# Kernel tuning notes

Hardware: AMD Instinct MI355X
Metric: run time of the kernel (lower is better)

## Reference

```python
import jax, jax.numpy as jnp
import numpy as np

S, B, H, T = 1024, 32, 1024, 512


def setup_inputs() -> dict:
    key = jax.random.key(0)
    ks = jax.random.split(key, 7)
    scale = 1.0 / np.sqrt(H)
    return {
        "hidden": jax.random.normal(ks[0], (S, B, H), dtype=jnp.float32),
        "x": jax.random.normal(ks[1], (B, T, H), dtype=jnp.float32),
        "problem_q": jax.random.normal(ks[2], (B, H), dtype=jnp.float32),
        "K_w": jax.random.normal(ks[3], (H, H), dtype=jnp.float32) * scale,
        "K_b": jax.random.normal(ks[4], (H,), dtype=jnp.float32) * scale,
        "V_w": jax.random.normal(ks[5], (H, H), dtype=jnp.float32) * scale,
        "V_b": jax.random.normal(ks[6], (H,), dtype=jnp.float32) * scale,
    }


def reference(hidden, x, problem_q, K_w, K_b, V_w, V_b):
    # hidden: [S, B, H] -> hidden2: [B, S, H]
    hidden2 = jnp.transpose(hidden, (1, 0, 2))
    # Linear projections (torch Linear: y = x @ W.T + b)
    k = jnp.einsum("bsh,kh->bsk", hidden2, K_w) + K_b  # [B, S, H]
    v = jnp.einsum("bsh,kh->bsk", hidden2, V_w) + V_b  # [B, S, H]
    # scores[b,t,s] = x[b,t] . k[b,s]  (QK^T per batch)
    scores = jnp.einsum("bth,bsh->bts", x, k)
    attn = jax.nn.softmax(scores, axis=-1)  # softmax over encoder positions S
    out = jax.nn.sigmoid(jnp.einsum("bts,bsh->bth", attn, v))  # [B, T, H]
    return out
```

## Files before the change

kernel.cpp:

```cpp
#include <hip/hip_runtime.h>

typedef unsigned short u16;
typedef __attribute__((ext_vector_type(8))) short short8;
typedef __attribute__((ext_vector_type(4))) float f32x4;
typedef __attribute__((ext_vector_type(4))) u16 u16x4;
typedef __attribute__((ext_vector_type(4))) unsigned int u32x4;

#define DEVINL static __device__ __forceinline__

DEVINL u16 f2bf(float f) {
  unsigned u = __builtin_bit_cast(unsigned, f);
  u += 0x7fffu + ((u >> 16) & 1u);
  return (u16)(u >> 16);
}
DEVINL float bf2f(u16 h) {
  return __builtin_bit_cast(float, ((unsigned)h) << 16);
}

DEVINL void gload16(const void* g, void* l) {
  __builtin_amdgcn_global_load_lds(
      (const __attribute__((address_space(1))) void*)g,
      (__attribute__((address_space(3))) void*)l, 16, 0, 0);
}

#define BAR() asm volatile("s_barrier" ::: "memory")
#define WAIT_VM0() asm volatile("s_waitcnt vmcnt(0)" ::: "memory")
#define WAIT_LGKM0() asm volatile("s_waitcnt lgkmcnt(0)" ::: "memory")


__global__ __launch_bounds__(256) void cvt_hidden3_k(const float* __restrict__ hid,
                                                     u16* __restrict__ hhi,
                                                     u16* __restrict__ hlo,
                                                     u16* __restrict__ hT) {
  __shared__ u16 tl[64][72];
  const int s0 = blockIdx.x * 64;
  const int h0 = blockIdx.y * 64;
  const int b = blockIdx.z;
  const int t = threadIdx.x;
  const int r = t >> 4;
  const int c4 = (t & 15) * 4;
#pragma unroll
  for (int it = 0; it < 4; ++it) {
    const int s = it * 16 + r;
    const f32x4 v = *(const f32x4*)(hid + ((size_t)(s0 + s) * 32 + b) * 1024 + h0 + c4);
    u16x4 oh, ol;
#pragma unroll
    for (int j = 0; j < 4; ++j) {
      const u16 hv = f2bf(v[j]);
      oh[j] = hv;
      ol[j] = f2bf(v[j] - bf2f(hv));
      tl[s][c4 + j] = hv;
    }
    const size_t base = ((size_t)b * 1024 + s0 + s) * 1024 + h0 + c4;
    *(u16x4*)(hhi + base) = oh;
    *(u16x4*)(hlo + base) = ol;
  }
  __syncthreads();
  const int h = t >> 2;
  const int sq = (t & 3) * 16;
  u16 tmp[16] __attribute__((aligned(16)));
#pragma unroll
  for (int i = 0; i < 16; ++i) tmp[i] = tl[sq + i][h];
  u16* dst = hT + ((size_t)b * 1024 + h0 + h) * 1024 + s0 + sq;
  *(u32x4*)(dst) = *(const u32x4*)&tmp[0];
  *(u32x4*)(dst + 8) = *(const u32x4*)&tmp[8];
}

__global__ __launch_bounds__(256) void cvt_split_k(const float* __restrict__ in,
                                                   u16* __restrict__ hi_o,
                                                   u16* __restrict__ lo_o, long n4) {
  long i = (long)blockIdx.x * 256 + threadIdx.x;
  const long stride = (long)gridDim.x * 256;
  for (; i < n4; i += stride) {
    const f32x4 v = ((const f32x4*)in)[i];
    u16x4 oh, ol;
#pragma unroll
    for (int j = 0; j < 4; ++j) {
      const u16 hi = f2bf(v[j]);
      oh[j] = hi;
      ol[j] = f2bf(v[j] - bf2f(hi));
    }
    ((u16x4*)hi_o)[i] = oh;
    ((u16x4*)lo_o)[i] = ol;
  }
}

__global__ __launch_bounds__(256) void cvt_f32_bf16_k(const float* __restrict__ in,
                                                      u16* __restrict__ out, long n4) {
  long i = (long)blockIdx.x * 256 + threadIdx.x;
  const long stride = (long)gridDim.x * 256;
  for (; i < n4; i += stride) {
    const f32x4 v = ((const f32x4*)in)[i];
    u16x4 o;
#pragma unroll
    for (int j = 0; j < 4; ++j) o[j] = f2bf(v[j]);
    ((u16x4*)out)[i] = o;
  }
}

__global__ __launch_bounds__(256) void cvt_w_split_t_k(const float* __restrict__ in,
                                                       u16* __restrict__ hi_o,
                                                       u16* __restrict__ lo_o) {
  __shared__ float tile[64][65];
  const int bh = blockIdx.x * 64;
  const int bj = blockIdx.y * 64;
  const int t = threadIdx.x;
  const int r = t >> 4;
  const int c4 = (t & 15) * 4;
#pragma unroll
  for (int it = 0; it < 4; ++it) {
    const int row = it * 16 + r;
    const f32x4 v = *(const f32x4*)(in + (size_t)(bj + row) * 1024 + bh + c4);
#pragma unroll
    for (int j = 0; j < 4; ++j) tile[c4 + j][row] = v[j];
  }
  __syncthreads();
#pragma unroll
  for (int it = 0; it < 4; ++it) {
    const int hrow = it * 16 + r;
    u16x4 oh, ol;
#pragma unroll
    for (int j = 0; j < 4; ++j) {
      const float f = tile[hrow][c4 + j];
      const u16 hv = f2bf(f);
      oh[j] = hv;
      ol[j] = f2bf(f - bf2f(hv));
    }
    *(u16x4*)(hi_o + (size_t)(bh + hrow) * 1024 + bj + c4) = oh;
    *(u16x4*)(lo_o + (size_t)(bh + hrow) * 1024 + bj + c4) = ol;
  }
}

template <int CMODE>
__global__ __launch_bounds__(512) void gemm3_8ph_k(
    const u16* __restrict__ Ah_, const u16* __restrict__ Al_,
    const u16* __restrict__ Bh_, const u16* __restrict__ Bl_,
    void* __restrict__ C0, void* __restrict__ C1) {
  __shared__ u16 lds[2][2][256 * 64];
  const int bid = blockIdx.x;
  const int swz = (bid & 7) * 32 + (bid >> 3);
  int m0, n0;
  const u16 *Ah, *Al, *Bh, *Bl;
  float* Cf = nullptr;
  u16 *Chi = nullptr, *Clo = nullptr;
  if (CMODE == 0) {
    m0 = (swz >> 2) * 256;
    n0 = (swz & 3) * 256;
    Ah = Ah_; Al = Al_; Bh = Bh_; Bl = Bl_;
    Chi = (u16*)C0; Clo = (u16*)C1;
  } else {
    const int z = swz >> 3;
    m0 = ((swz >> 2) & 1) * 256;
    n0 = (swz & 3) * 256;
    Ah = Ah_ + (size_t)z * 512 * 1024;  Al = Al_ + (size_t)z * 512 * 1024;
    Bh = Bh_ + (size_t)z * 1024 * 1024; Bl = Bl_ + (size_t)z * 1024 * 1024;
    Cf = (float*)C0 + (size_t)z * 512 * 1024;
  }
  const int tid = threadIdx.x;
  const int lane = tid & 63, wid = tid >> 6;
  const int wr = wid >> 2, wc = wid & 3;
  const int fr = lane & 15, fk = lane >> 4;

  f32x4 acc[8][4] = {};

#define STAGE3(pb, q, gph, gpl, rb, kt)                                        \
  {                                                                            \
    _Pragma("unroll") for (int j = 0; j < 4; ++j) {                            \
      const int slot = j * 512 + tid;                                          \
      const int r = slot >> 3;                                                 \
      const int g = (slot & 7) ^ (r & 7);                                      \
      const u16* src = (g < 4) ? (gph) : (gpl);                                \
      gload16(src + (size_t)((rb) + r) * 1024 + (kt) * 32 + (g & 3) * 8,       \
              &lds[pb][q][(j * 512 + wid * 64) * 8]);                          \
    }                                                                          \
  }

  STAGE3(0, 0, Ah, Al, m0, 0);
  STAGE3(0, 1, Bh, Bl, n0, 0);

  for (int t = 0; t < 32; ++t) {
    const int p = t & 1;
    WAIT_VM0();
    BAR();
    short8 bh[4], bl[4];
#pragma unroll
    for (int ph = 0; ph < 4; ++ph) {
      short8 ah[2], al[2];
#pragma unroll
      for (int i = 0; i < 2; ++i) {
        const int r = wr * 128 + (ph * 2 + i) * 16 + fr;
        const int ch = fk ^ (r & 7);
        ah[i] = *(const short8*)&lds[p][0][r * 64 + ch * 8];
        al[i] = *(const short8*)&lds[p][0][r * 64 + (ch ^ 4) * 8];
      }
      if (ph == 0) {
#pragma unroll
        for (int nf = 0; nf < 4; ++nf) {
          const int rn = wc * 64 + nf * 16 + fr;
          const int cn = fk ^ (rn & 7);
          bh[nf] = *(const short8*)&lds[p][1][rn * 64 + cn * 8];
          bl[nf] = *(const short8*)&lds[p][1][rn * 64 + (cn ^ 4) * 8];
        }
        if (t < 31) STAGE3(p ^ 1, 0, Ah, Al, m0, t + 1);
      }
      if (ph == 1 && t < 31) STAGE3(p ^ 1, 1, Bh, Bl, n0, t + 1);
      BAR();
      WAIT_LGKM0();
      __builtin_amdgcn_sched_barrier(0);
      __builtin_amdgcn_s_setprio(1);
#pragma unroll
      for (int i = 0; i < 2; ++i)
#pragma unroll
        for (int nf = 0; nf < 4; ++nf) {
          acc[ph * 2 + i][nf] =
              __builtin_amdgcn_mfma_f32_16x16x32_bf16(ah[i], bh[nf], acc[ph * 2 + i][nf], 0, 0, 0);
          acc[ph * 2 + i][nf] =
              __builtin_amdgcn_mfma_f32_16x16x32_bf16(ah[i], bl[nf], acc[ph * 2 + i][nf], 0, 0, 0);
          acc[ph * 2 + i][nf] =
              __builtin_amdgcn_mfma_f32_16x16x32_bf16(al[i], bh[nf], acc[ph * 2 + i][nf], 0, 0, 0);
        }
      __builtin_amdgcn_s_setprio(0);
      BAR();
    }
  }
#undef STAGE3

  const int cb = n0 + wc * 64 + fr;
  const int rb = m0 + wr * 128 + fk * 4;
  if (CMODE == 0) {
#pragma unroll
    for (int mf = 0; mf < 8; ++mf)
#pragma unroll
      for (int nf = 0; nf < 4; ++nf) {
        const int col = cb + nf * 16;
#pragma unroll
        for (int j = 0; j < 4; ++j) {
          const int row = rb + mf * 16 + j;
          const float kv = acc[mf][nf][j];
          const u16 hi = f2bf(kv);
          Chi[(size_t)row * 1024 + col] = hi;
          Clo[(size_t)row * 1024 + col] = f2bf(kv - bf2f(hi));
        }
      }
  } else {
#pragma unroll
    for (int mf = 0; mf < 8; ++mf)
#pragma unroll
      for (int nf = 0; nf < 4; ++nf) {
        const int col = cb + nf * 16;
#pragma unroll
        for (int j = 0; j < 4; ++j) {
          const int row = rb + mf * 16 + j;
          Cf[(size_t)row * 1024 + col] = acc[mf][nf][j];
        }
      }
  }
}

template <int CM>
__global__ __launch_bounds__(512) void gemm1_8ph_k(
    const u16* __restrict__ A_, const u16* __restrict__ Bt_,
    const float* __restrict__ bias, void* __restrict__ Cout) {
  __shared__ u16 lds[2][2][256 * 64];
  const int bid = blockIdx.x;
  const int swz = (bid & 7) * 32 + (bid >> 3);
  int m0, n0;
  const u16 *A, *Bt;
  float* Cf = nullptr;
  u16* Cb = nullptr;
  if (CM == 0) {
    const int z = swz >> 3;
    m0 = ((swz >> 2) & 1) * 256;
    n0 = (swz & 3) * 256;
    A = A_ + (size_t)z * 512 * 1024;
    Bt = Bt_ + (size_t)z * 1024 * 1024;
    Cb = (u16*)Cout + (size_t)z * 512 * 1024;
  } else {
    m0 = (swz >> 2) * 256;
    n0 = (swz & 3) * 256;
    A = A_; Bt = Bt_;
    Cf = (float*)Cout;
  }
  const int tid = threadIdx.x;
  const int lane = tid & 63, wid = tid >> 6;
  const int wr = wid >> 2, wc = wid & 3;
  const int fr = lane & 15, fk = lane >> 4;

  f32x4 acc[8][4] = {};

#define STAGE1(pb, q, gp, rb, kt)                                              \
  {                                                                            \
    _Pragma("unroll") for (int j = 0; j < 4; ++j) {                            \
      const int slot = j * 512 + tid;                                          \
      const int r = slot >> 3;                                                 \
      const int g = (slot & 7) ^ (r & 7);                                      \
      gload16((gp) + (size_t)((rb) + r) * 1024 + (kt) * 64 + g * 8,            \
              &lds[pb][q][(j * 512 + wid * 64) * 8]);                          \
    }                                                                          \
  }

  STAGE1(0, 0, A, m0, 0);
  STAGE1(0, 1, Bt, n0, 0);

  for (int t = 0; t < 16; ++t) {
    const int p = t & 1;
    WAIT_VM0();
    BAR();
    short8 bfr[4][2];
#pragma unroll
    for (int ph = 0; ph < 4; ++ph) {
      short8 a[2][2];
#pragma unroll
      for (int i = 0; i < 2; ++i) {
        const int r = wr * 128 + (ph * 2 + i) * 16 + fr;
#pragma unroll
        for (int ks = 0; ks < 2; ++ks) {
          const int g = (ks * 4 + fk) ^ (r & 7);
          a[i][ks] = *(const short8*)&lds[p][0][r * 64 + g * 8];
        }
      }
      if (ph == 0) {
#pragma unroll
        for (int nf = 0; nf < 4; ++nf) {
          const int rn = wc * 64 + nf * 16 + fr;
#pragma unroll
          for (int ks = 0; ks < 2; ++ks) {
            const int g = (ks * 4 + fk) ^ (rn & 7);
            bfr[nf][ks] = *(const short8*)&lds[p][1][rn * 64 + g * 8];
          }
        }
        if (t < 15) {
          STAGE1(p ^ 1, 0, A, m0, t + 1);
          STAGE1(p ^ 1, 1, Bt, n0, t + 1);
        }
      }
      BAR();
      WAIT_LGKM0();
      __builtin_amdgcn_sched_barrier(0);
      __builtin_amdgcn_s_setprio(1);
#pragma unroll
      for (int i = 0; i < 2; ++i)
#pragma unroll
        for (int nf = 0; nf < 4; ++nf) {
          acc[ph * 2 + i][nf] = __builtin_amdgcn_mfma_f32_16x16x32_bf16(
              a[i][0], bfr[nf][0], acc[ph * 2 + i][nf], 0, 0, 0);
          acc[ph * 2 + i][nf] = __builtin_amdgcn_mfma_f32_16x16x32_bf16(
              a[i][1], bfr[nf][1], acc[ph * 2 + i][nf], 0, 0, 0);
        }
      __builtin_amdgcn_s_setprio(0);
      BAR();
    }
  }
#undef STAGE1

  const int cb = n0 + wc * 64 + fr;
  const int rb = m0 + wr * 128 + fk * 4;
  if (CM == 0) {
#pragma unroll
    for (int mf = 0; mf < 8; ++mf)
#pragma unroll
      for (int nf = 0; nf < 4; ++nf) {
        const int col = cb + nf * 16;
#pragma unroll
        for (int j = 0; j < 4; ++j) {
          const int row = rb + mf * 16 + j;
          Cb[(size_t)row * 1024 + col] = f2bf(acc[mf][nf][j]);
        }
      }
  } else {
#pragma unroll
    for (int mf = 0; mf < 8; ++mf)
#pragma unroll
      for (int nf = 0; nf < 4; ++nf) {
        const int col = cb + nf * 16;
        const float bv = bias[col];
#pragma unroll
        for (int j = 0; j < 4; ++j) {
          const int row = rb + mf * 16 + j;
          const float xv = acc[mf][nf][j] + bv;
          Cf[(size_t)row * 1024 + col] = 1.0f / (1.0f + __expf(-xv));
        }
      }
  }
}

__global__ __launch_bounds__(256) void softmax_k(const float* __restrict__ S,
                                                 u16* __restrict__ Attn) {
  const float* rp = S + (size_t)blockIdx.x * 1024;
  const int tid = threadIdx.x;
  const int lane = tid & 63, wid = tid >> 6;
  const f32x4 v = ((const f32x4*)rp)[tid];
  float mx = fmaxf(fmaxf(v[0], v[1]), fmaxf(v[2], v[3]));
#pragma unroll
  for (int off = 32; off; off >>= 1) mx = fmaxf(mx, __shfl_xor(mx, off));
  __shared__ float red[4];
  __shared__ float red2[4];
  if (lane == 0) red[wid] = mx;
  __syncthreads();
  mx = fmaxf(fmaxf(red[0], red[1]), fmaxf(red[2], red[3]));
  const float e0 = __expf(v[0] - mx), e1 = __expf(v[1] - mx);
  const float e2 = __expf(v[2] - mx), e3 = __expf(v[3] - mx);
  float s = (e0 + e1) + (e2 + e3);
#pragma unroll
  for (int off = 32; off; off >>= 1) s += __shfl_xor(s, off);
  if (lane == 0) red2[wid] = s;
  __syncthreads();
  const float inv = 1.0f / (red2[0] + red2[1] + red2[2] + red2[3]);
  u16x4 o;
  o[0] = f2bf(e0 * inv); o[1] = f2bf(e1 * inv); o[2] = f2bf(e2 * inv); o[3] = f2bf(e3 * inv);
  ((u16x4*)(Attn + (size_t)blockIdx.x * 1024))[tid] = o;
}

extern "C" void kernel_launch(void* const* d_in, const int* in_sizes, int n_in,
                              void* d_out, int out_size, void* d_ws, size_t ws_size,
                              hipStream_t stream) {
  const float* hidden = (const float*)d_in[0];
  const float* x = (const float*)d_in[1];
  const float* K_w = (const float*)d_in[3];
  const float* V_w = (const float*)d_in[5];
  const float* V_b = (const float*)d_in[6];

  char* ws = (char*)d_ws;
  u16* hhi = (u16*)(ws);
  u16* hlo = (u16*)(ws + 67108864);
  u16* hT  = (u16*)(ws + 134217728);
  u16* qhi = (u16*)(ws + 201326592);
  u16* qlo = (u16*)(ws + 234881024);
  float* scoresF = (float*)(ws + 268435456);
  u16* attn = qhi;
  u16* ctx = hhi;
  u16* kwt_h = (u16*)(ws + 335544320);
  u16* kwt_l = kwt_h + 1024 * 1024;
  u16* vw = kwt_h + 2 * 1024 * 1024;
  u16* xhi = (u16*)d_out;
  u16* xlo = xhi + 32L * 512 * 1024;
  float* out = (float*)d_out;

  cvt_hidden3_k<<<dim3(16, 16, 32), 256, 0, stream>>>(hidden, hhi, hlo, hT);
  cvt_split_k<<<2048, 256, 0, stream>>>(x, xhi, xlo, 32L * 512 * 1024 / 4);
  cvt_w_split_t_k<<<dim3(16, 16), 256, 0, stream>>>(K_w, kwt_h, kwt_l);
  cvt_f32_bf16_k<<<1024, 256, 0, stream>>>(V_w, vw, 1024L * 1024 / 4);
  gemm3_8ph_k<0><<<256, 512, 0, stream>>>(xhi, xlo, kwt_h, kwt_l, qhi, qlo);
  gemm3_8ph_k<1><<<256, 512, 0, stream>>>(qhi, qlo, hhi, hlo, scoresF, nullptr);
  softmax_k<<<16384, 256, 0, stream>>>(scoresF, attn);
  gemm1_8ph_k<0><<<256, 512, 0, stream>>>(attn, hT, nullptr, ctx);
  gemm1_8ph_k<1><<<256, 512, 0, stream>>>(ctx, vw, V_b, out);
}
```

Before: 378.5 us.

## Use fp16 single-operand hidden and fp16 hi/lo query for score GEMM

The scores GEMM previously used a bf16 hi/lo split on both operands with three MFMAs per tile. Now hidden is converted once to fp16, dropping its low part, while the query product is split into fp16 hi/lo. A new gemm2 kernel issues two fp16 MFMAs per tile and loads half as much B data into LDS. This reduces the MFMA count, hidden conversion writes and global traffic for the largest GEMM, at the cost of fp16 range and precision on hidden and on q.

```diff
diff --git a/kernel.cpp b/kernel.cpp
--- a/kernel.cpp
+++ b/kernel.cpp
@@ -2,6 +2,7 @@
 
 typedef unsigned short u16;
 typedef __attribute__((ext_vector_type(8))) short short8;
+typedef __attribute__((ext_vector_type(8))) _Float16 half8;
 typedef __attribute__((ext_vector_type(4))) float f32x4;
 typedef __attribute__((ext_vector_type(4))) u16 u16x4;
 typedef __attribute__((ext_vector_type(4))) unsigned int u32x4;
@@ -16,6 +17,8 @@
 DEVINL float bf2f(u16 h) {
   return __builtin_bit_cast(float, ((unsigned)h) << 16);
 }
+DEVINL u16 f2h(float f) { return __builtin_bit_cast(u16, (_Float16)f); }
+DEVINL float h2f(u16 h) { return (float)__builtin_bit_cast(_Float16, h); }
 
 DEVINL void gload16(const void* g, void* l) {
   __builtin_amdgcn_global_load_lds(
@@ -28,9 +31,8 @@
 #define WAIT_LGKM0() asm volatile("s_waitcnt lgkmcnt(0)" ::: "memory")
 
 
-__global__ __launch_bounds__(256) void cvt_hidden3_k(const float* __restrict__ hid,
-                                                     u16* __restrict__ hhi,
-                                                     u16* __restrict__ hlo,
+__global__ __launch_bounds__(256) void cvt_hidden2_k(const float* __restrict__ hid,
+                                                     u16* __restrict__ hf,
                                                      u16* __restrict__ hT) {
   __shared__ u16 tl[64][72];
   const int s0 = blockIdx.x * 64;
@@ -43,17 +45,13 @@
   for (int it = 0; it < 4; ++it) {
     const int s = it * 16 + r;
     const f32x4 v = *(const f32x4*)(hid + ((size_t)(s0 + s) * 32 + b) * 1024 + h0 + c4);
-    u16x4 oh, ol;
+    u16x4 of;
 #pragma unroll
     for (int j = 0; j < 4; ++j) {
-      const u16 hv = f2bf(v[j]);
-      oh[j] = hv;
-      ol[j] = f2bf(v[j] - bf2f(hv));
-      tl[s][c4 + j] = hv;
-    }
-    const size_t base = ((size_t)b * 1024 + s0 + s) * 1024 + h0 + c4;
-    *(u16x4*)(hhi + base) = oh;
-    *(u16x4*)(hlo + base) = ol;
+      of[j] = f2h(v[j]);
+      tl[s][c4 + j] = f2bf(v[j]);
+    }
+    *(u16x4*)(hf + ((size_t)b * 1024 + s0 + s) * 1024 + h0 + c4) = of;
   }
   __syncthreads();
   const int h = t >> 2;
@@ -131,31 +129,15 @@
   }
 }
 
-template <int CMODE>
 __global__ __launch_bounds__(512) void gemm3_8ph_k(
-    const u16* __restrict__ Ah_, const u16* __restrict__ Al_,
-    const u16* __restrict__ Bh_, const u16* __restrict__ Bl_,
-    void* __restrict__ C0, void* __restrict__ C1) {
+    const u16* __restrict__ Ah, const u16* __restrict__ Al,
+    const u16* __restrict__ Bh, const u16* __restrict__ Bl,
+    u16* __restrict__ Chi, u16* __restrict__ Clo) {
   __shared__ u16 lds[2][2][256 * 64];
   const int bid = blockIdx.x;
   const int swz = (bid & 7) * 32 + (bid >> 3);
-  int m0, n0;
-  const u16 *Ah, *Al, *Bh, *Bl;
-  float* Cf = nullptr;
-  u16 *Chi = nullptr, *Clo = nullptr;
-  if (CMODE == 0) {
-    m0 = (swz >> 2) * 256;
-    n0 = (swz & 3) * 256;
-    Ah = Ah_; Al = Al_; Bh = Bh_; Bl = Bl_;
-    Chi = (u16*)C0; Clo = (u16*)C1;
-  } else {
-    const int z = swz >> 3;
-    m0 = ((swz >> 2) & 1) * 256;
-    n0 = (swz & 3) * 256;
-    Ah = Ah_ + (size_t)z * 512 * 1024;  Al = Al_ + (size_t)z * 512 * 1024;
-    Bh = Bh_ + (size_t)z * 1024 * 1024; Bl = Bl_ + (size_t)z * 1024 * 1024;
-    Cf = (float*)C0 + (size_t)z * 512 * 1024;
-  }
+  const int m0 = (swz >> 2) * 256;
+  const int n0 = (swz & 3) * 256;
   const int tid = threadIdx.x;
   const int lane = tid & 63, wid = tid >> 6;
   const int wr = wid >> 2, wc = wid & 3;
@@ -227,34 +209,126 @@
 
   const int cb = n0 + wc * 64 + fr;
   const int rb = m0 + wr * 128 + fk * 4;
-  if (CMODE == 0) {
-#pragma unroll
-    for (int mf = 0; mf < 8; ++mf)
-#pragma unroll
-      for (int nf = 0; nf < 4; ++nf) {
-        const int col = cb + nf * 16;
-#pragma unroll
-        for (int j = 0; j < 4; ++j) {
-          const int row = rb + mf * 16 + j;
-          const float kv = acc[mf][nf][j];
-          const u16 hi = f2bf(kv);
-          Chi[(size_t)row * 1024 + col] = hi;
-          Clo[(size_t)row * 1024 + col] = f2bf(kv - bf2f(hi));
-        }
-      }
-  } else {
-#pragma unroll
-    for (int mf = 0; mf < 8; ++mf)
-#pragma unroll
-      for (int nf = 0; nf < 4; ++nf) {
-        const int col = cb + nf * 16;
-#pragma unroll
-        for (int j = 0; j < 4; ++j) {
-          const int row = rb + mf * 16 + j;
-          Cf[(size_t)row * 1024 + col] = acc[mf][nf][j];
-        }
-      }
-  }
+#pragma unroll
+  for (int mf = 0; mf < 8; ++mf)
+#pragma unroll
+    for (int nf = 0; nf < 4; ++nf) {
+      const int col = cb + nf * 16;
+#pragma unroll
+      for (int j = 0; j < 4; ++j) {
+        const int row = rb + mf * 16 + j;
+        const float kv = acc[mf][nf][j];
+        const u16 hi = f2h(kv);
+        Chi[(size_t)row * 1024 + col] = hi;
+        Clo[(size_t)row * 1024 + col] = f2h(kv - h2f(hi));
+      }
+    }
+}
+
+__global__ __launch_bounds__(512) void gemm2_8ph_k(
+    const u16* __restrict__ Qh_, const u16* __restrict__ Ql_,
+    const u16* __restrict__ Hf_, float* __restrict__ S) {
+  __shared__ u16 lA[2][256 * 64];
+  __shared__ u16 lB[2][256 * 32];
+  const int bid = blockIdx.x;
+  const int swz = (bid & 7) * 32 + (bid >> 3);
+  const int z = swz >> 3;
+  const int m0 = ((swz >> 2) & 1) * 256;
+  const int n0 = (swz & 3) * 256;
+  const u16* Qh = Qh_ + (size_t)z * 512 * 1024;
+  const u16* Ql = Ql_ + (size_t)z * 512 * 1024;
+  const u16* Hf = Hf_ + (size_t)z * 1024 * 1024;
+  float* Cf = S + (size_t)z * 512 * 1024;
+  const int tid = threadIdx.x;
+  const int lane = tid & 63, wid = tid >> 6;
+  const int wr = wid >> 2, wc = wid & 3;
+  const int fr = lane & 15, fk = lane >> 4;
+
+  f32x4 acc[8][4] = {};
+
+#define STAGEA(pb, kt)                                                         \
+  {                                                                            \
+    _Pragma("unroll") for (int j = 0; j < 4; ++j) {                            \
+      const int slot = j * 512 + tid;                                          \
+      const int r = slot >> 3;                                                 \
+      const int g = (slot & 7) ^ (r & 7);                                      \
+      const u16* src = (g < 4) ? Qh : Ql;                                      \
+      gload16(src + (size_t)(m0 + r) * 1024 + (kt) * 32 + (g & 3) * 8,         \
+              &lA[pb][(j * 512 + wid * 64) * 8]);                              \
+    }                                                                          \
+  }
+#define STAGEB(pb, kt)                                                         \
+  {                                                                            \
+    _Pragma("unroll") for (int j = 0; j < 2; ++j) {                            \
+      const int slot = j * 512 + tid;                                          \
+      const int r = slot >> 2;                                                 \
+      const int g = (slot & 3) ^ ((r >> 1) & 3);                               \
+      gload16(Hf + (size_t)(n0 + r) * 1024 + (kt) * 32 + g * 8,                \
+              &lB[pb][(j * 512 + wid * 64) * 8]);                              \
+    }                                                                          \
+  }
+
+  STAGEA(0, 0);
+  STAGEB(0, 0);
+
+  for (int t = 0; t < 32; ++t) {
+    const int p = t & 1;
+    WAIT_VM0();
+    BAR();
+    half8 bf[4];
+#pragma unroll
+    for (int ph = 0; ph < 4; ++ph) {
+      half8 ah[2], al[2];
+#pragma unroll
+      for (int i = 0; i < 2; ++i) {
+        const int r = wr * 128 + (ph * 2 + i) * 16 + fr;
+        const int ch = fk ^ (r & 7);
+        ah[i] = *(const half8*)&lA[p][r * 64 + ch * 8];
+        al[i] = *(const half8*)&lA[p][r * 64 + (ch ^ 4) * 8];
+      }
+      if (ph == 0) {
+#pragma unroll
+        for (int nf = 0; nf < 4; ++nf) {
+          const int rn = wc * 64 + nf * 16 + fr;
+          const int cn = fk ^ ((rn >> 1) & 3);
+          bf[nf] = *(const half8*)&lB[p][rn * 32 + cn * 8];
+        }
+        if (t < 31) STAGEA(p ^ 1, t + 1);
+      }
+      if (ph == 1 && t < 31) STAGEB(p ^ 1, t + 1);
+      BAR();
+      WAIT_LGKM0();
+      __builtin_amdgcn_sched_barrier(0);
+      __builtin_amdgcn_s_setprio(1);
+#pragma unroll
+      for (int i = 0; i < 2; ++i)
+#pragma unroll
+        for (int nf = 0; nf < 4; ++nf) {
+          acc[ph * 2 + i][nf] =
+              __builtin_amdgcn_mfma_f32_16x16x32_f16(ah[i], bf[nf], acc[ph * 2 + i][nf], 0, 0, 0);
+          acc[ph * 2 + i][nf] =
+              __builtin_amdgcn_mfma_f32_16x16x32_f16(al[i], bf[nf], acc[ph * 2 + i][nf], 0, 0, 0);
+        }
+      __builtin_amdgcn_s_setprio(0);
+      BAR();
+    }
+  }
+#undef STAGEA
+#undef STAGEB
+
+  const int cb = n0 + wc * 64 + fr;
+  const int rb = m0 + wr * 128 + fk * 4;
+#pragma unroll
+  for (int mf = 0; mf < 8; ++mf)
+#pragma unroll
+    for (int nf = 0; nf < 4; ++nf) {
+      const int col = cb + nf * 16;
+#pragma unroll
+      for (int j = 0; j < 4; ++j) {
+        const int row = rb + mf * 16 + j;
+        Cf[(size_t)row * 1024 + col] = acc[mf][nf][j];
+      }
+    }
 }
 
 template <int CM>
@@ -421,27 +495,26 @@
   const float* V_b = (const float*)d_in[6];
 
   char* ws = (char*)d_ws;
-  u16* hhi = (u16*)(ws);
-  u16* hlo = (u16*)(ws + 67108864);
-  u16* hT  = (u16*)(ws + 134217728);
-  u16* qhi = (u16*)(ws + 201326592);
-  u16* qlo = (u16*)(ws + 234881024);
-  float* scoresF = (float*)(ws + 268435456);
-  u16* attn = qhi;
-  u16* ctx = hhi;
-  u16* kwt_h = (u16*)(ws + 335544320);
+  u16* hf16 = (u16*)(ws);
+  u16* hT = (u16*)(ws + 67108864);
+  u16* qhi = (u16*)(ws + 134217728);
+  u16* qlo = (u16*)(ws + 167772160);
+  float* scoresF = (float*)(ws + 201326592);
+  u16* attn = hf16;
+  u16* ctx = qhi;
+  u16* kwt_h = (u16*)(ws + 268435456);
   u16* kwt_l = kwt_h + 1024 * 1024;
   u16* vw = kwt_h + 2 * 1024 * 1024;
   u16* xhi = (u16*)d_out;
   u16* xlo = xhi + 32L * 512 * 1024;
   float* out = (float*)d_out;
 
-  cvt_hidden3_k<<<dim3(16, 16, 32), 256, 0, stream>>>(hidden, hhi, hlo, hT);
+  cvt_hidden2_k<<<dim3(16, 16, 32), 256, 0, stream>>>(hidden, hf16, hT);
   cvt_split_k<<<2048, 256, 0, stream>>>(x, xhi, xlo, 32L * 512 * 1024 / 4);
   cvt_w_split_t_k<<<dim3(16, 16), 256, 0, stream>>>(K_w, kwt_h, kwt_l);
   cvt_f32_bf16_k<<<1024, 256, 0, stream>>>(V_w, vw, 1024L * 1024 / 4);
-  gemm3_8ph_k<0><<<256, 512, 0, stream>>>(xhi, xlo, kwt_h, kwt_l, qhi, qlo);
-  gemm3_8ph_k<1><<<256, 512, 0, stream>>>(qhi, qlo, hhi, hlo, scoresF, nullptr);
+  gemm3_8ph_k<<<256, 512, 0, stream>>>(xhi, xlo, kwt_h, kwt_l, qhi, qlo);
+  gemm2_8ph_k<<<256, 512, 0, stream>>>(qhi, qlo, hf16, scoresF);
   softmax_k<<<16384, 256, 0, stream>>>(scoresF, attn);
   gemm1_8ph_k<0><<<256, 512, 0, stream>>>(attn, hT, nullptr, ctx);
   gemm1_8ph_k<1><<<256, 512, 0, stream>>>(ctx, vw, V_b, out);
```

New measurement: 349.4 us. 7.7% less time.
